# Kernel tuning notes

Hardware: AMD Instinct MI355X
Metric: run time of the kernel (lower is better)

Reference implementation:

```python
import jax, jax.numpy as jnp
import numpy as np


def setup_inputs() -> dict:
    key = jax.random.key(0)
    kq, kk, kv = jax.random.split(key, 3)
    B, H, T, D = 2, 8, 8192, 64
    return {
        "Q": jax.random.normal(kq, (B, H, T, D), dtype=jnp.float32),
        "K": jax.random.normal(kk, (B, H, T, D), dtype=jnp.float32),
        "V": jax.random.normal(kv, (B, H, T, D), dtype=jnp.float32),
        "window_size": 512,
    }


def _gather_bands(x, nb, Wn):
    # x: [B,H,T,D] -> [B,H,nb,3*Wn,D], key blocks (i-1, i, i+1) per query block i
    B, H, T, D = x.shape
    xb = x.reshape(B, H, nb, Wn, D)
    xp = jnp.pad(xb, ((0, 0), (0, 0), (1, 1), (0, 0), (0, 0)))
    return jnp.concatenate([xp[:, :, i:i + nb] for i in range(3)], axis=3)


def reference(Q, K, V, window_size):
    # Sliding-window attention: softmax over keys with |q_idx - kv_idx| <= window_size,
    # computed block-sparsely (only the 3 neighboring key blocks per query block).
    B, H, T, D = Q.shape
    Wn = int(window_size)
    assert T % Wn == 0
    nb = T // Wn
    scale = 1.0 / (D ** 0.5)

    Qb = Q.reshape(B, H, nb, Wn, D)
    Kw = _gather_bands(K, nb, Wn)  # [B,H,nb,3W,D]
    Vw = _gather_bands(V, nb, Wn)

    # scores within the band: [B,H,nb,W,3W]
    s = jnp.einsum('bhnqd,bhnkd->bhnqk', Qb, Kw) * scale

    # exact band mask: global q = n*W + q_loc, global kv = (n-1)*W + k_loc
    q_loc = jnp.arange(Wn)[:, None]
    k_loc = jnp.arange(3 * Wn)[None, :]
    band = jnp.abs(q_loc + Wn - k_loc) <= Wn          # [W, 3W]
    kv_g = (jnp.arange(nb)[:, None] - 1) * Wn + jnp.arange(3 * Wn)[None, :]  # [nb, 3W]
    valid = (kv_g >= 0) & (kv_g < T)
    mask = band[None, :, :] & valid[:, None, :]        # [nb, W, 3W]

    s = jnp.where(mask[None, None], s, -jnp.inf)
    p = jax.nn.softmax(s, axis=-1)
    o = jnp.einsum('bhnqk,bhnkd->bhnqd', p, Vw)
    return o.reshape(B, H, T, D)
```

## Files before the change

### kernel.cpp

```cpp
#include <hip/hip_runtime.h>
#include <hip/hip_bf16.h>
#include <stdint.h>

typedef __attribute__((ext_vector_type(8))) short bf16x8;
typedef __attribute__((ext_vector_type(4))) short bf16x4;
typedef __attribute__((ext_vector_type(4))) float f32x4;

#define T_SEQ   8192
#define D_HEAD  64
#define NHEADS  16
#define WIN     512
#define BQ      128
#define BK      64
#define NTILES  (T_SEQ / BK)
#define LDSR    72
#define MASKVAL (-1.0e6f)

#define WS_NEEDED ((size_t)2 * NHEADS * T_SEQ * D_HEAD * 2)

#define MFMA16(a,b,c) __builtin_amdgcn_mfma_f32_16x16x16bf16_1k(a,b,c,0,0,0)

__device__ __forceinline__ short f2bf(float f) {
    union { float f; uint32_t u; } v; v.f = f;
    return (short)((v.u + 0x7FFFu + ((v.u >> 16) & 1u)) >> 16);
}

__device__ __forceinline__ uint32_t pkbf2(float lo, float hi) {
    union { __hip_bfloat162 h; uint32_t u; } c;
    c.h = __float22bfloat162_rn(make_float2(lo, hi));
    return c.u;
}

__global__ __launch_bounds__(256, 2)
void prep_kv(const float* __restrict__ Kg, const float* __restrict__ Vg,
             short* __restrict__ Kb, short* __restrict__ Vt)
{
    __shared__ float vt[64 * 65];
    const int tid  = threadIdx.x;
    const int tile = blockIdx.x & (NTILES - 1);
    const int head = blockIdx.x >> 7;
    const size_t off = ((size_t)head * T_SEQ + (size_t)tile * BK) * D_HEAD;

    const float* ks = Kg + off;
    short* kd = Kb + off;
    #pragma unroll
    for (int i = 0; i < 4; ++i) {
        int idx = tid + 256 * i;
        float4 v = *(const float4*)(ks + idx * 4);
        short4 h = { f2bf(v.x), f2bf(v.y), f2bf(v.z), f2bf(v.w) };
        *(short4*)(kd + idx * 4) = h;
    }

    const float* vs = Vg + off;
    #pragma unroll
    for (int i = 0; i < 4; ++i) {
        int idx = tid + 256 * i;
        int row = idx >> 4, c4 = (idx & 15) << 2;
        float4 v = *(const float4*)(vs + row * D_HEAD + c4);
        *(float4*)&vt[row * 65 + c4] = v;
    }
    __syncthreads();
    short* vd = Vt + ((size_t)head * NTILES + tile) * (BK * D_HEAD);
    {
        int d = tid >> 2, kq = (tid & 3) << 4;
        short out[16];
        #pragma unroll
        for (int j = 0; j < 16; ++j) out[j] = f2bf(vt[(kq + j) * 65 + d]);
        *(bf16x8*)(vd + d * BK + kq)     = *(bf16x8*)&out[0];
        *(bf16x8*)(vd + d * BK + kq + 8) = *(bf16x8*)&out[8];
    }
}

__global__ __launch_bounds__(256, 4)
void swa_fwd(const float* __restrict__ Qg, const short* __restrict__ Kb,
             const short* __restrict__ Vt, float* __restrict__ Og)
{
    __shared__ short Ks[BK * LDSR];
    __shared__ short Vs[D_HEAD * LDSR];

    const int tid  = threadIdx.x;
    const int wave = tid >> 6;
    const int lane = tid & 63;
    const int lcol = lane & 15;
    const int quad = lane >> 4;

    const int g    = blockIdx.x;
    const int head = (g >> 3) >> 3;
    const int qt   = ((g & 7) << 3) | ((g >> 3) & 7);
    const int q0   = qt * BQ;
    const int tq   = q0 >> 6;

    const float* Qp = Qg + (size_t)head * T_SEQ * D_HEAD;
    const short* Kp = Kb + (size_t)head * T_SEQ * D_HEAD;
    float*       Op = Og + (size_t)head * T_SEQ * D_HEAD;

    const float qscale = 0.125f * 1.44269504088896340736f;
    const int qrow_w = q0 + wave * 32;

    bf16x8 qf[2][2];
    #pragma unroll
    for (int mt = 0; mt < 2; ++mt) {
        const float* qptr = Qp + (size_t)(qrow_w + mt*16 + lcol) * D_HEAD + quad * 8;
        #pragma unroll
        for (int ks = 0; ks < 2; ++ks) {
            float4 a = *(const float4*)(qptr + ks*32);
            float4 b = *(const float4*)(qptr + ks*32 + 4);
            bf16x8 f;
            f[0]=f2bf(a.x*qscale); f[1]=f2bf(a.y*qscale); f[2]=f2bf(a.z*qscale); f[3]=f2bf(a.w*qscale);
            f[4]=f2bf(b.x*qscale); f[5]=f2bf(b.y*qscale); f[6]=f2bf(b.z*qscale); f[7]=f2bf(b.w*qscale);
            qf[mt][ks] = f;
        }
    }

    f32x4 oacc[2][4];
    float l_run[2];
    const f32x4 zero4 = {0.f, 0.f, 0.f, 0.f};
    #pragma unroll
    for (int mt = 0; mt < 2; ++mt) {
        l_run[mt] = 0.f;
        #pragma unroll
        for (int nt = 0; nt < 4; ++nt) oacc[mt][nt] = zero4;
    }

    int t0 = (q0 - WIN) >> 6;            if (t0 < 0) t0 = 0;
    int t1 = (q0 + BQ - 1 + WIN) >> 6;   if (t1 > NTILES - 1) t1 = NTILES - 1;

    for (int t = t0; t <= t1; ++t) {
        __syncthreads();
        {
            const short* ksrc = Kp + (size_t)t * BK * D_HEAD;
            const short* vsrc = Vt + ((size_t)head * NTILES + t) * (BK * D_HEAD);
            #pragma unroll
            for (int i = 0; i < 2; ++i) {
                int idx = tid + 256 * i;
                int row = idx >> 3, c = (idx & 7) << 3;
                *(bf16x8*)&Ks[row * LDSR + c] = *(const bf16x8*)(ksrc + idx * 8);
                *(bf16x8*)&Vs[row * LDSR + c] = *(const bf16x8*)(vsrc + idx * 8);
            }
        }
        __syncthreads();

        const bool edge = (t < tq - 6) || (t > tq + 7);

        #pragma unroll
        for (int h = 0; h < 2; ++h) {
            f32x4 sc[2][2];
            #pragma unroll
            for (int j = 0; j < 2; ++j) { sc[j][0] = zero4; sc[j][1] = zero4; }
            #pragma unroll
            for (int ks = 0; ks < 2; ++ks) {
                #pragma unroll
                for (int j = 0; j < 2; ++j) {
                    bf16x8 kf = *(const bf16x8*)&Ks[((2*h+j)*16 + lcol)*LDSR + ks*32 + quad*8];
                    sc[j][0] = __builtin_amdgcn_mfma_f32_16x16x32_bf16(kf, qf[0][ks], sc[j][0], 0,0,0);
                    sc[j][1] = __builtin_amdgcn_mfma_f32_16x16x32_bf16(kf, qf[1][ks], sc[j][1], 0,0,0);
                }
            }

            if (edge) {
                #pragma unroll
                for (int j = 0; j < 2; ++j) {
                    const int kg0 = t*BK + (2*h+j)*16 + quad*4;
                    #pragma unroll
                    for (int mt = 0; mt < 2; ++mt) {
                        const int qg = qrow_w + mt*16 + lcol;
                        #pragma unroll
                        for (int r = 0; r < 4; ++r) {
                            int dq = qg - (kg0 + r);
                            if (dq > WIN || dq < -WIN) sc[j][mt][r] = MASKVAL;
                        }
                    }
                }
            }

            #pragma unroll
            for (int j = 0; j < 2; ++j) {
                const int kt = 2*h + j;
                bf16x4 vf[4];
                #pragma unroll
                for (int nt = 0; nt < 4; ++nt)
                    vf[nt] = *(const bf16x4*)&Vs[(nt*16 + lcol)*LDSR + kt*16 + quad*4];
                #pragma unroll
                for (int mt = 0; mt < 2; ++mt) {
                    float p0 = exp2f(sc[j][mt][0]);
                    float p1 = exp2f(sc[j][mt][1]);
                    float p2 = exp2f(sc[j][mt][2]);
                    float p3 = exp2f(sc[j][mt][3]);
                    l_run[mt] += (p0 + p1) + (p2 + p3);
                    union { int2 i; bf16x4 v; } pf;
                    pf.i = make_int2((int)pkbf2(p0, p1), (int)pkbf2(p2, p3));
                    #pragma unroll
                    for (int nt = 0; nt < 4; ++nt)
                        oacc[mt][nt] = MFMA16(vf[nt], pf.v, oacc[mt][nt]);
                }
            }
        }
    }

    #pragma unroll
    for (int mt = 0; mt < 2; ++mt) {
        float l = l_run[mt];
        l += __shfl_xor(l, 16, 64);
        l += __shfl_xor(l, 32, 64);
        float inv = 1.0f / l;
        const int qg = qrow_w + mt*16 + lcol;
        float* op = Op + (size_t)qg * D_HEAD + quad*4;
        #pragma unroll
        for (int nt = 0; nt < 4; ++nt) {
            float4 o = { oacc[mt][nt][0]*inv, oacc[mt][nt][1]*inv,
                         oacc[mt][nt][2]*inv, oacc[mt][nt][3]*inv };
            *(float4*)(op + nt*16) = o;
        }
    }
}

#define M_INIT  (-1.0e4f)
__global__ __launch_bounds__(256, 2)
void swa_fwd_fb(const float* __restrict__ Qg, const float* __restrict__ Kg,
                const float* __restrict__ Vg, float* __restrict__ Og)
{
    __shared__ short Ks[BK * LDSR];
    __shared__ short Vs[D_HEAD * LDSR];
    __shared__ short Ps[4 * 32 * LDSR];

    const int tid  = threadIdx.x;
    const int wave = tid >> 6;
    const int lane = tid & 63;
    const int lcol = lane & 15;
    const int quad = lane >> 4;

    const int g    = blockIdx.x;
    const int head = (g >> 3) >> 3;
    const int qt   = ((g & 7) << 3) | ((g >> 3) & 7);
    const int q0   = qt * BQ;

    const size_t base = (size_t)head * T_SEQ * D_HEAD;
    const float* Qp = Qg + base;
    const float* Kp = Kg + base;
    const float* Vp = Vg + base;
    float*       Op = Og + base;

    const float qscale = 0.125f * 1.44269504088896340736f;
    const int qrow_w = q0 + wave * 32;

    bf16x8 qf[2][2];
    #pragma unroll
    for (int mt = 0; mt < 2; ++mt) {
        const float* qptr = Qp + (size_t)(qrow_w + mt*16 + lcol) * D_HEAD + quad * 8;
        #pragma unroll
        for (int ks = 0; ks < 2; ++ks) {
            float4 a = *(const float4*)(qptr + ks*32);
            float4 b = *(const float4*)(qptr + ks*32 + 4);
            bf16x8 f;
            f[0]=f2bf(a.x*qscale); f[1]=f2bf(a.y*qscale); f[2]=f2bf(a.z*qscale); f[3]=f2bf(a.w*qscale);
            f[4]=f2bf(b.x*qscale); f[5]=f2bf(b.y*qscale); f[6]=f2bf(b.z*qscale); f[7]=f2bf(b.w*qscale);
            qf[mt][ks] = f;
        }
    }

    f32x4 oacc[2][4];
    float m_run[2][4], l_run[2][4];
    const f32x4 zero4 = {0.f, 0.f, 0.f, 0.f};
    #pragma unroll
    for (int mt = 0; mt < 2; ++mt) {
        #pragma unroll
        for (int r = 0; r < 4; ++r) { m_run[mt][r] = M_INIT; l_run[mt][r] = 0.f; }
        #pragma unroll
        for (int nt = 0; nt < 4; ++nt) oacc[mt][nt] = zero4;
    }

    int t0 = (q0 - WIN) >> 6;            if (t0 < 0) t0 = 0;
    int t1 = (q0 + BQ - 1 + WIN) >> 6;   if (t1 > NTILES - 1) t1 = NTILES - 1;

    for (int t = t0; t <= t1; ++t) {
        __syncthreads();
        {
            const float* src = Kp + (size_t)t * BK * D_HEAD;
            #pragma unroll
            for (int i = 0; i < 4; ++i) {
                int f4 = tid + 256*i;
                int row = f4 >> 4, c4 = (f4 & 15) << 2;
                float4 v = *(const float4*)(src + row*D_HEAD + c4);
                short4 h = { f2bf(v.x), f2bf(v.y), f2bf(v.z), f2bf(v.w) };
                *(short4*)&Ks[row*LDSR + c4] = h;
            }
            const float* vsrc = Vp + (size_t)t * BK * D_HEAD;
            int col = tid & 63, rb = (tid >> 6) << 2;
            #pragma unroll
            for (int i = 0; i < 4; ++i) {
                int r = rb + 16*i;
                short4 h = { f2bf(vsrc[(r+0)*D_HEAD + col]),
                             f2bf(vsrc[(r+1)*D_HEAD + col]),
                             f2bf(vsrc[(r+2)*D_HEAD + col]),
                             f2bf(vsrc[(r+3)*D_HEAD + col]) };
                *(short4*)&Vs[col*LDSR + r] = h;
            }
        }
        __syncthreads();

        f32x4 sc[2][4];
        #pragma unroll
        for (int mt = 0; mt < 2; ++mt)
            #pragma unroll
            for (int kt = 0; kt < 4; ++kt) sc[mt][kt] = zero4;
        #pragma unroll
        for (int kt = 0; kt < 4; ++kt) {
            #pragma unroll
            for (int ks = 0; ks < 2; ++ks) {
                bf16x8 kf = *(const bf16x8*)&Ks[(kt*16 + lcol)*LDSR + ks*32 + quad*8];
                sc[0][kt] = __builtin_amdgcn_mfma_f32_16x16x32_bf16(qf[0][ks], kf, sc[0][kt], 0,0,0);
                sc[1][kt] = __builtin_amdgcn_mfma_f32_16x16x32_bf16(qf[1][ks], kf, sc[1][kt], 0,0,0);
            }
        }

        const int kb = t * BK + lcol;
        #pragma unroll
        for (int mt = 0; mt < 2; ++mt) {
            const int qrow = qrow_w + mt*16 + quad*4;
            #pragma unroll
            for (int kt = 0; kt < 4; ++kt) {
                int kg = kb + kt*16;
                #pragma unroll
                for (int r = 0; r < 4; ++r) {
                    int dq = (qrow + r) - kg;
                    if (dq > WIN || dq < -WIN) sc[mt][kt][r] = MASKVAL;
                }
            }
            float tm[4], al[4], rs[4];
            #pragma unroll
            for (int r = 0; r < 4; ++r)
                tm[r] = fmaxf(fmaxf(sc[mt][0][r], sc[mt][1][r]), fmaxf(sc[mt][2][r], sc[mt][3][r]));
            #pragma unroll
            for (int off = 1; off < 16; off <<= 1)
                #pragma unroll
                for (int r = 0; r < 4; ++r)
                    tm[r] = fmaxf(tm[r], __shfl_xor(tm[r], off, 64));
            #pragma unroll
            for (int r = 0; r < 4; ++r) {
                float mn = fmaxf(m_run[mt][r], tm[r]);
                al[r] = exp2f(m_run[mt][r] - mn);
                m_run[mt][r] = mn;
                rs[r] = 0.f;
            }
            #pragma unroll
            for (int kt = 0; kt < 4; ++kt)
                #pragma unroll
                for (int r = 0; r < 4; ++r) {
                    float p = exp2f(sc[mt][kt][r] - m_run[mt][r]);
                    sc[mt][kt][r] = p;
                    rs[r] += p;
                }
            #pragma unroll
            for (int off = 1; off < 16; off <<= 1)
                #pragma unroll
                for (int r = 0; r < 4; ++r)
                    rs[r] += __shfl_xor(rs[r], off, 64);
            #pragma unroll
            for (int r = 0; r < 4; ++r)
                l_run[mt][r] = l_run[mt][r]*al[r] + rs[r];
            #pragma unroll
            for (int nt = 0; nt < 4; ++nt)
                #pragma unroll
                for (int r = 0; r < 4; ++r) oacc[mt][nt][r] *= al[r];
            short* pw = &Ps[(wave*32 + mt*16 + quad*4) * LDSR];
            #pragma unroll
            for (int kt = 0; kt < 4; ++kt)
                #pragma unroll
                for (int r = 0; r < 4; ++r)
                    pw[r*LDSR + kt*16 + lcol] = f2bf(sc[mt][kt][r]);
        }

        const short* pr = &Ps[wave*32*LDSR];
        #pragma unroll
        for (int ks = 0; ks < 2; ++ks) {
            bf16x8 pf0 = *(const bf16x8*)&pr[(lcol     )*LDSR + ks*32 + quad*8];
            bf16x8 pf1 = *(const bf16x8*)&pr[(16 + lcol)*LDSR + ks*32 + quad*8];
            #pragma unroll
            for (int nt = 0; nt < 4; ++nt) {
                bf16x8 vf = *(const bf16x8*)&Vs[(nt*16 + lcol)*LDSR + ks*32 + quad*8];
                oacc[0][nt] = __builtin_amdgcn_mfma_f32_16x16x32_bf16(pf0, vf, oacc[0][nt], 0,0,0);
                oacc[1][nt] = __builtin_amdgcn_mfma_f32_16x16x32_bf16(pf1, vf, oacc[1][nt], 0,0,0);
            }
        }
    }

    #pragma unroll
    for (int mt = 0; mt < 2; ++mt)
        #pragma unroll
        for (int r = 0; r < 4; ++r) {
            int row = qrow_w + mt*16 + quad*4 + r;
            float inv = 1.0f / l_run[mt][r];
            float* op = Op + (size_t)row * D_HEAD + lcol;
            #pragma unroll
            for (int nt = 0; nt < 4; ++nt)
                op[nt*16] = oacc[mt][nt][r] * inv;
        }
}

extern "C" void kernel_launch(void* const* d_in, const int* in_sizes, int n_in,
                              void* d_out, int out_size, void* d_ws, size_t ws_size,
                              hipStream_t stream)
{
    const float* Q = (const float*)d_in[0];
    const float* K = (const float*)d_in[1];
    const float* V = (const float*)d_in[2];
    float* O = (float*)d_out;

    if (ws_size >= WS_NEEDED) {
        short* Kb = (short*)d_ws;
        short* Vt = Kb + (size_t)NHEADS * T_SEQ * D_HEAD;
        prep_kv<<<dim3(NHEADS * NTILES), dim3(256), 0, stream>>>(K, V, Kb, Vt);
        swa_fwd<<<dim3(NHEADS * (T_SEQ / BQ)), dim3(256), 0, stream>>>(Q, Kb, Vt, O);
    } else {
        swa_fwd_fb<<<dim3(NHEADS * (T_SEQ / BQ)), dim3(256), 0, stream>>>(Q, K, V, O);
    }
}
```

Baseline: 199.6 us.

## Fuse K/V bf16 conversion and V transpose into the attention kernel

Removes the separate prep_kv pass and converts fp32 K/V tiles to bf16 inside the attention loop, transposing V through an fp32 LDS staging buffer. Global loads are issued before the barrier so they can overlap with prior work, and exp2f is replaced by the native exp2 intrinsic. This drops one launch and the workspace round trip. In exchange, each K/V tile is now converted about 18 times, once per overlapping query block, and extra LDS, a third barrier and more registers may reduce occupancy. The fallback kernel is deleted.

```diff
diff --git a/kernel.cpp b/kernel.cpp
--- a/kernel.cpp
+++ b/kernel.cpp
@@ -14,11 +14,13 @@
 #define BK      64
 #define NTILES  (T_SEQ / BK)
 #define LDSR    72
+#define VTR     65
 #define MASKVAL (-1.0e6f)
 
-#define WS_NEEDED ((size_t)2 * NHEADS * T_SEQ * D_HEAD * 2)
-
 #define MFMA16(a,b,c) __builtin_amdgcn_mfma_f32_16x16x16bf16_1k(a,b,c,0,0,0)
+
+extern "C" __device__ __attribute__((const)) float __ocml_native_exp2_f32(float);
+__device__ __forceinline__ float fexp2(float x) { return __ocml_native_exp2_f32(x); }
 
 __device__ __forceinline__ short f2bf(float f) {
     union { float f; uint32_t u; } v; v.f = f;
@@ -31,52 +33,13 @@
     return c.u;
 }
 
-__global__ __launch_bounds__(256, 2)
-void prep_kv(const float* __restrict__ Kg, const float* __restrict__ Vg,
-             short* __restrict__ Kb, short* __restrict__ Vt)
-{
-    __shared__ float vt[64 * 65];
-    const int tid  = threadIdx.x;
-    const int tile = blockIdx.x & (NTILES - 1);
-    const int head = blockIdx.x >> 7;
-    const size_t off = ((size_t)head * T_SEQ + (size_t)tile * BK) * D_HEAD;
-
-    const float* ks = Kg + off;
-    short* kd = Kb + off;
-    #pragma unroll
-    for (int i = 0; i < 4; ++i) {
-        int idx = tid + 256 * i;
-        float4 v = *(const float4*)(ks + idx * 4);
-        short4 h = { f2bf(v.x), f2bf(v.y), f2bf(v.z), f2bf(v.w) };
-        *(short4*)(kd + idx * 4) = h;
-    }
-
-    const float* vs = Vg + off;
-    #pragma unroll
-    for (int i = 0; i < 4; ++i) {
-        int idx = tid + 256 * i;
-        int row = idx >> 4, c4 = (idx & 15) << 2;
-        float4 v = *(const float4*)(vs + row * D_HEAD + c4);
-        *(float4*)&vt[row * 65 + c4] = v;
-    }
-    __syncthreads();
-    short* vd = Vt + ((size_t)head * NTILES + tile) * (BK * D_HEAD);
-    {
-        int d = tid >> 2, kq = (tid & 3) << 4;
-        short out[16];
-        #pragma unroll
-        for (int j = 0; j < 16; ++j) out[j] = f2bf(vt[(kq + j) * 65 + d]);
-        *(bf16x8*)(vd + d * BK + kq)     = *(bf16x8*)&out[0];
-        *(bf16x8*)(vd + d * BK + kq + 8) = *(bf16x8*)&out[8];
-    }
-}
-
 __global__ __launch_bounds__(256, 4)
-void swa_fwd(const float* __restrict__ Qg, const short* __restrict__ Kb,
-             const short* __restrict__ Vt, float* __restrict__ Og)
+void swa_fused(const float* __restrict__ Qg, const float* __restrict__ Kg,
+               const float* __restrict__ Vg, float* __restrict__ Og)
 {
     __shared__ short Ks[BK * LDSR];
     __shared__ short Vs[D_HEAD * LDSR];
+    __shared__ float Vtmp[BK * VTR];
 
     const int tid  = threadIdx.x;
     const int wave = tid >> 6;
@@ -85,14 +48,16 @@
     const int quad = lane >> 4;
 
     const int g    = blockIdx.x;
-    const int head = (g >> 3) >> 3;
+    const int head = g >> 6;
     const int qt   = ((g & 7) << 3) | ((g >> 3) & 7);
     const int q0   = qt * BQ;
     const int tq   = q0 >> 6;
 
-    const float* Qp = Qg + (size_t)head * T_SEQ * D_HEAD;
-    const short* Kp = Kb + (size_t)head * T_SEQ * D_HEAD;
-    float*       Op = Og + (size_t)head * T_SEQ * D_HEAD;
+    const size_t hoff = (size_t)head * T_SEQ * D_HEAD;
+    const float* Qp = Qg + hoff;
+    const float* Kp = Kg + hoff;
+    const float* Vp = Vg + hoff;
+    float*       Op = Og + hoff;
 
     const float qscale = 0.125f * 1.44269504088896340736f;
     const int qrow_w = q0 + wave * 32;
@@ -125,19 +90,49 @@
     int t0 = (q0 - WIN) >> 6;            if (t0 < 0) t0 = 0;
     int t1 = (q0 + BQ - 1 + WIN) >> 6;   if (t1 > NTILES - 1) t1 = NTILES - 1;
 
+    const int krow0 = tid >> 3, kc = (tid & 7) << 3;
+    const int krow1 = krow0 + 32;
+    const int vrow  = tid >> 4, vc = (tid & 15) << 2;
+    const int td    = tid >> 2, tkq = (tid & 3) << 4;
+
     for (int t = t0; t <= t1; ++t) {
+        const float* ksrc = Kp + (size_t)t * BK * D_HEAD;
+        const float* vsrc = Vp + (size_t)t * BK * D_HEAD;
+        float4 k00 = *(const float4*)(ksrc + krow0*D_HEAD + kc);
+        float4 k01 = *(const float4*)(ksrc + krow0*D_HEAD + kc + 4);
+        float4 k10 = *(const float4*)(ksrc + krow1*D_HEAD + kc);
+        float4 k11 = *(const float4*)(ksrc + krow1*D_HEAD + kc + 4);
+        float4 v0  = *(const float4*)(vsrc + (vrow     )*D_HEAD + vc);
+        float4 v1  = *(const float4*)(vsrc + (vrow + 16)*D_HEAD + vc);
+        float4 v2  = *(const float4*)(vsrc + (vrow + 32)*D_HEAD + vc);
+        float4 v3  = *(const float4*)(vsrc + (vrow + 48)*D_HEAD + vc);
+
         __syncthreads();
+
+        *(float4*)&Vtmp[(vrow     )*VTR + vc] = v0;
+        *(float4*)&Vtmp[(vrow + 16)*VTR + vc] = v1;
+        *(float4*)&Vtmp[(vrow + 32)*VTR + vc] = v2;
+        *(float4*)&Vtmp[(vrow + 48)*VTR + vc] = v3;
+        *(int4*)&Ks[krow0*LDSR + kc] = make_int4((int)pkbf2(k00.x,k00.y), (int)pkbf2(k00.z,k00.w),
+                                                 (int)pkbf2(k01.x,k01.y), (int)pkbf2(k01.z,k01.w));
+        *(int4*)&Ks[krow1*LDSR + kc] = make_int4((int)pkbf2(k10.x,k10.y), (int)pkbf2(k10.z,k10.w),
+                                                 (int)pkbf2(k11.x,k11.y), (int)pkbf2(k11.z,k11.w));
+
+        __syncthreads();
+
         {
-            const short* ksrc = Kp + (size_t)t * BK * D_HEAD;
-            const short* vsrc = Vt + ((size_t)head * NTILES + t) * (BK * D_HEAD);
-            #pragma unroll
-            for (int i = 0; i < 2; ++i) {
-                int idx = tid + 256 * i;
-                int row = idx >> 3, c = (idx & 7) << 3;
-                *(bf16x8*)&Ks[row * LDSR + c] = *(const bf16x8*)(ksrc + idx * 8);
-                *(bf16x8*)&Vs[row * LDSR + c] = *(const bf16x8*)(vsrc + idx * 8);
-            }
-        }
+            uint32_t w0 = pkbf2(Vtmp[(tkq+ 0)*VTR + td], Vtmp[(tkq+ 1)*VTR + td]);
+            uint32_t w1 = pkbf2(Vtmp[(tkq+ 2)*VTR + td], Vtmp[(tkq+ 3)*VTR + td]);
+            uint32_t w2 = pkbf2(Vtmp[(tkq+ 4)*VTR + td], Vtmp[(tkq+ 5)*VTR + td]);
+            uint32_t w3 = pkbf2(Vtmp[(tkq+ 6)*VTR + td], Vtmp[(tkq+ 7)*VTR + td]);
+            uint32_t w4 = pkbf2(Vtmp[(tkq+ 8)*VTR + td], Vtmp[(tkq+ 9)*VTR + td]);
+            uint32_t w5 = pkbf2(Vtmp[(tkq+10)*VTR + td], Vtmp[(tkq+11)*VTR + td]);
+            uint32_t w6 = pkbf2(Vtmp[(tkq+12)*VTR + td], Vtmp[(tkq+13)*VTR + td]);
+            uint32_t w7 = pkbf2(Vtmp[(tkq+14)*VTR + td], Vtmp[(tkq+15)*VTR + td]);
+            *(int4*)&Vs[td*LDSR + tkq]     = make_int4((int)w0,(int)w1,(int)w2,(int)w3);
+            *(int4*)&Vs[td*LDSR + tkq + 8] = make_int4((int)w4,(int)w5,(int)w6,(int)w7);
+        }
+
         __syncthreads();
 
         const bool edge = (t < tq - 6) || (t > tq + 7);
@@ -182,10 +177,10 @@
                     vf[nt] = *(const bf16x4*)&Vs[(nt*16 + lcol)*LDSR + kt*16 + quad*4];
                 #pragma unroll
                 for (int mt = 0; mt < 2; ++mt) {
-                    float p0 = exp2f(sc[j][mt][0]);
-                    float p1 = exp2f(sc[j][mt][1]);
-                    float p2 = exp2f(sc[j][mt][2]);
-                    float p3 = exp2f(sc[j][mt][3]);
+                    float p0 = fexp2(sc[j][mt][0]);
+                    float p1 = fexp2(sc[j][mt][1]);
+                    float p2 = fexp2(sc[j][mt][2]);
+                    float p3 = fexp2(sc[j][mt][3]);
                     l_run[mt] += (p0 + p1) + (p2 + p3);
                     union { int2 i; bf16x4 v; } pf;
                     pf.i = make_int2((int)pkbf2(p0, p1), (int)pkbf2(p2, p3));
@@ -214,204 +209,14 @@
     }
 }
 
-#define M_INIT  (-1.0e4f)
-__global__ __launch_bounds__(256, 2)
-void swa_fwd_fb(const float* __restrict__ Qg, const float* __restrict__ Kg,
-                const float* __restrict__ Vg, float* __restrict__ Og)
-{
-    __shared__ short Ks[BK * LDSR];
-    __shared__ short Vs[D_HEAD * LDSR];
-    __shared__ short Ps[4 * 32 * LDSR];
-
-    const int tid  = threadIdx.x;
-    const int wave = tid >> 6;
-    const int lane = tid & 63;
-    const int lcol = lane & 15;
-    const int quad = lane >> 4;
-
-    const int g    = blockIdx.x;
-    const int head = (g >> 3) >> 3;
-    const int qt   = ((g & 7) << 3) | ((g >> 3) & 7);
-    const int q0   = qt * BQ;
-
-    const size_t base = (size_t)head * T_SEQ * D_HEAD;
-    const float* Qp = Qg + base;
-    const float* Kp = Kg + base;
-    const float* Vp = Vg + base;
-    float*       Op = Og + base;
-
-    const float qscale = 0.125f * 1.44269504088896340736f;
-    const int qrow_w = q0 + wave * 32;
-
-    bf16x8 qf[2][2];
-    #pragma unroll
-    for (int mt = 0; mt < 2; ++mt) {
-        const float* qptr = Qp + (size_t)(qrow_w + mt*16 + lcol) * D_HEAD + quad * 8;
-        #pragma unroll
-        for (int ks = 0; ks < 2; ++ks) {
-            float4 a = *(const float4*)(qptr + ks*32);
-            float4 b = *(const float4*)(qptr + ks*32 + 4);
-            bf16x8 f;
-            f[0]=f2bf(a.x*qscale); f[1]=f2bf(a.y*qscale); f[2]=f2bf(a.z*qscale); f[3]=f2bf(a.w*qscale);
-            f[4]=f2bf(b.x*qscale); f[5]=f2bf(b.y*qscale); f[6]=f2bf(b.z*qscale); f[7]=f2bf(b.w*qscale);
-            qf[mt][ks] = f;
-        }
-    }
-
-    f32x4 oacc[2][4];
-    float m_run[2][4], l_run[2][4];
-    const f32x4 zero4 = {0.f, 0.f, 0.f, 0.f};
-    #pragma unroll
-    for (int mt = 0; mt < 2; ++mt) {
-        #pragma unroll
-        for (int r = 0; r < 4; ++r) { m_run[mt][r] = M_INIT; l_run[mt][r] = 0.f; }
-        #pragma unroll
-        for (int nt = 0; nt < 4; ++nt) oacc[mt][nt] = zero4;
-    }
-
-    int t0 = (q0 - WIN) >> 6;            if (t0 < 0) t0 = 0;
-    int t1 = (q0 + BQ - 1 + WIN) >> 6;   if (t1 > NTILES - 1) t1 = NTILES - 1;
-
-    for (int t = t0; t <= t1; ++t) {
-        __syncthreads();
-        {
-            const float* src = Kp + (size_t)t * BK * D_HEAD;
-            #pragma unroll
-            for (int i = 0; i < 4; ++i) {
-                int f4 = tid + 256*i;
-                int row = f4 >> 4, c4 = (f4 & 15) << 2;
-                float4 v = *(const float4*)(src + row*D_HEAD + c4);
-                short4 h = { f2bf(v.x), f2bf(v.y), f2bf(v.z), f2bf(v.w) };
-                *(short4*)&Ks[row*LDSR + c4] = h;
-            }
-            const float* vsrc = Vp + (size_t)t * BK * D_HEAD;
-            int col = tid & 63, rb = (tid >> 6) << 2;
-            #pragma unroll
-            for (int i = 0; i < 4; ++i) {
-                int r = rb + 16*i;
-                short4 h = { f2bf(vsrc[(r+0)*D_HEAD + col]),
-                             f2bf(vsrc[(r+1)*D_HEAD + col]),
-                             f2bf(vsrc[(r+2)*D_HEAD + col]),
-                             f2bf(vsrc[(r+3)*D_HEAD + col]) };
-                *(short4*)&Vs[col*LDSR + r] = h;
-            }
-        }
-        __syncthreads();
-
-        f32x4 sc[2][4];
-        #pragma unroll
-        for (int mt = 0; mt < 2; ++mt)
-            #pragma unroll
-            for (int kt = 0; kt < 4; ++kt) sc[mt][kt] = zero4;
-        #pragma unroll
-        for (int kt = 0; kt < 4; ++kt) {
-            #pragma unroll
-            for (int ks = 0; ks < 2; ++ks) {
-                bf16x8 kf = *(const bf16x8*)&Ks[(kt*16 + lcol)*LDSR + ks*32 + quad*8];
-                sc[0][kt] = __builtin_amdgcn_mfma_f32_16x16x32_bf16(qf[0][ks], kf, sc[0][kt], 0,0,0);
-                sc[1][kt] = __builtin_amdgcn_mfma_f32_16x16x32_bf16(qf[1][ks], kf, sc[1][kt], 0,0,0);
-            }
-        }
-
-        const int kb = t * BK + lcol;
-        #pragma unroll
-        for (int mt = 0; mt < 2; ++mt) {
-            const int qrow = qrow_w + mt*16 + quad*4;
-            #pragma unroll
-            for (int kt = 0; kt < 4; ++kt) {
-                int kg = kb + kt*16;
-                #pragma unroll
-                for (int r = 0; r < 4; ++r) {
-                    int dq = (qrow + r) - kg;
-                    if (dq > WIN || dq < -WIN) sc[mt][kt][r] = MASKVAL;
-                }
-            }
-            float tm[4], al[4], rs[4];
-            #pragma unroll
-            for (int r = 0; r < 4; ++r)
-                tm[r] = fmaxf(fmaxf(sc[mt][0][r], sc[mt][1][r]), fmaxf(sc[mt][2][r], sc[mt][3][r]));
-            #pragma unroll
-            for (int off = 1; off < 16; off <<= 1)
-                #pragma unroll
-                for (int r = 0; r < 4; ++r)
-                    tm[r] = fmaxf(tm[r], __shfl_xor(tm[r], off, 64));
-            #pragma unroll
-            for (int r = 0; r < 4; ++r) {
-                float mn = fmaxf(m_run[mt][r], tm[r]);
-                al[r] = exp2f(m_run[mt][r] - mn);
-                m_run[mt][r] = mn;
-                rs[r] = 0.f;
-            }
-            #pragma unroll
-            for (int kt = 0; kt < 4; ++kt)
-                #pragma unroll
-                for (int r = 0; r < 4; ++r) {
-                    float p = exp2f(sc[mt][kt][r] - m_run[mt][r]);
-                    sc[mt][kt][r] = p;
-                    rs[r] += p;
-                }
-            #pragma unroll
-            for (int off = 1; off < 16; off <<= 1)
-                #pragma unroll
-                for (int r = 0; r < 4; ++r)
-                    rs[r] += __shfl_xor(rs[r], off, 64);
-            #pragma unroll
-            for (int r = 0; r < 4; ++r)
-                l_run[mt][r] = l_run[mt][r]*al[r] + rs[r];
-            #pragma unroll
-            for (int nt = 0; nt < 4; ++nt)
-                #pragma unroll
-                for (int r = 0; r < 4; ++r) oacc[mt][nt][r] *= al[r];
-            short* pw = &Ps[(wave*32 + mt*16 + quad*4) * LDSR];
-            #pragma unroll
-            for (int kt = 0; kt < 4; ++kt)
-                #pragma unroll
-                for (int r = 0; r < 4; ++r)
-                    pw[r*LDSR + kt*16 + lcol] = f2bf(sc[mt][kt][r]);
-        }
-
-        const short* pr = &Ps[wave*32*LDSR];
-        #pragma unroll
-        for (int ks = 0; ks < 2; ++ks) {
-            bf16x8 pf0 = *(const bf16x8*)&pr[(lcol     )*LDSR + ks*32 + quad*8];
-            bf16x8 pf1 = *(const bf16x8*)&pr[(16 + lcol)*LDSR + ks*32 + quad*8];
-            #pragma unroll
-            for (int nt = 0; nt < 4; ++nt) {
-                bf16x8 vf = *(const bf16x8*)&Vs[(nt*16 + lcol)*LDSR + ks*32 + quad*8];
-                oacc[0][nt] = __builtin_amdgcn_mfma_f32_16x16x32_bf16(pf0, vf, oacc[0][nt], 0,0,0);
-                oacc[1][nt] = __builtin_amdgcn_mfma_f32_16x16x32_bf16(pf1, vf, oacc[1][nt], 0,0,0);
-            }
-        }
-    }
-
-    #pragma unroll
-    for (int mt = 0; mt < 2; ++mt)
-        #pragma unroll
-        for (int r = 0; r < 4; ++r) {
-            int row = qrow_w + mt*16 + quad*4 + r;
-            float inv = 1.0f / l_run[mt][r];
-            float* op = Op + (size_t)row * D_HEAD + lcol;
-            #pragma unroll
-            for (int nt = 0; nt < 4; ++nt)
-                op[nt*16] = oacc[mt][nt][r] * inv;
-        }
-}
-
 extern "C" void kernel_launch(void* const* d_in, const int* in_sizes, int n_in,
                               void* d_out, int out_size, void* d_ws, size_t ws_size,
                               hipStream_t stream)
 {
+    (void)in_sizes; (void)n_in; (void)out_size; (void)d_ws; (void)ws_size;
     const float* Q = (const float*)d_in[0];
     const float* K = (const float*)d_in[1];
     const float* V = (const float*)d_in[2];
     float* O = (float*)d_out;
-
-    if (ws_size >= WS_NEEDED) {
-        short* Kb = (short*)d_ws;
-        short* Vt = Kb + (size_t)NHEADS * T_SEQ * D_HEAD;
-        prep_kv<<<dim3(NHEADS * NTILES), dim3(256), 0, stream>>>(K, V, Kb, Vt);
-        swa_fwd<<<dim3(NHEADS * (T_SEQ / BQ)), dim3(256), 0, stream>>>(Q, Kb, Vt, O);
-    } else {
-        swa_fwd_fb<<<dim3(NHEADS * (T_SEQ / BQ)), dim3(256), 0, stream>>>(Q, K, V, O);
-    }
-}
+    swa_fused<<<dim3(NHEADS * (T_SEQ / BQ)), dim3(256), 0, stream>>>(Q, K, V, O);
+}
```

After: 202.9 us. No clear change (+1.7%).
